# Kernel optimization log

Measured on AMD Instinct MI355X. Metric: run time of the kernel, lower is better.

Reference implementation:

```python
import jax, jax.numpy as jnp
import numpy as np

N, E, DIN, DOUT = 30000, 480000, 512, 512


def setup_inputs() -> dict:
    key = jax.random.key(0)
    ks = jax.random.split(key, 20)
    inp = {}
    inp["x"] = jax.random.normal(ks[0], (N, DIN), jnp.float32)
    inp["edge_index"] = jax.random.randint(ks[1], (2, E), 0, N, dtype=jnp.int64)
    inp["edge_weight"] = jax.random.uniform(ks[2], (E,), jnp.float32)
    sc = 1.0 / np.sqrt(DIN)
    sl = 1.0 / np.sqrt(2 * DOUT)
    for i, g in enumerate(["i", "f", "g", "o"]):
        inp[f"Wc_{g}"] = jax.random.normal(ks[3 + 4 * i], (DIN, DOUT), jnp.float32) * sc
        inp[f"bc_{g}"] = jnp.zeros((DOUT,), jnp.float32)
        inp[f"Wl_{g}"] = jax.random.normal(ks[4 + 4 * i], (2 * DOUT, DOUT), jnp.float32) * sl
        inp[f"bl_{g}"] = jnp.zeros((DOUT,), jnp.float32)
    return inp


def _gcn_norm(src, dst, w, n):
    # add self loops with weight 1.0 (improved=False), then symmetric normalization
    loops = jnp.arange(n, dtype=src.dtype)
    src = jnp.concatenate([src, loops])
    dst = jnp.concatenate([dst, loops])
    w = jnp.concatenate([w, jnp.ones((n,), w.dtype)])
    deg = jax.ops.segment_sum(w, dst, num_segments=n)
    dinv = jnp.where(deg > 0, jax.lax.rsqrt(jnp.where(deg > 0, deg, 1.0)), 0.0)
    norm = dinv[src] * w * dinv[dst]
    return src, dst, norm


def reference(x, edge_index, edge_weight,
              Wc_i, bc_i, Wl_i, bl_i,
              Wc_f, bc_f, Wl_f, bl_f,
              Wc_g, bc_g, Wl_g, bl_g,
              Wc_o, bc_o, Wl_o, bl_o):
    n = x.shape[0]
    src, dst, norm = _gcn_norm(edge_index[0], edge_index[1], edge_weight, n)
    H = jnp.zeros((n, DOUT), x.dtype)  # _set_hidden_state default
    C = jnp.zeros((n, DOUT), x.dtype)  # _set_cell_state default

    def conv(Wc, bc):
        xw = x @ Wc                                        # [N, DOUT] dense GEMM
        agg = jax.ops.segment_sum(norm[:, None] * xw[src], dst, num_segments=n)
        return agg + bc

    def gate(Wc, bc, Wl, bl, act):
        z = jnp.concatenate([conv(Wc, bc), H], axis=1)      # [N, 2*DOUT]
        return act(z @ Wl + bl)

    I = gate(Wc_i, bc_i, Wl_i, bl_i, jax.nn.sigmoid)
    F = gate(Wc_f, bc_f, Wl_f, bl_f, jax.nn.sigmoid)
    G = gate(Wc_g, bc_g, Wl_g, bl_g, jnp.tanh)
    O = gate(Wc_o, bc_o, Wl_o, bl_o, jax.nn.sigmoid)
    Cn = F * C + I * G
    Hn = O * jnp.tanh(Cn)
    return O, Hn, Cn
```

## Files before the change

kernel.cpp:

```cpp
#include <hip/hip_runtime.h>
#include <stdint.h>

typedef __bf16 bf16;
typedef __attribute__((ext_vector_type(4))) float f4;
typedef __attribute__((ext_vector_type(4))) float f32x4;
typedef __attribute__((ext_vector_type(8))) __bf16 bf8v;
typedef __attribute__((ext_vector_type(4))) __bf16 bf4v;

#define NN 30000
#define MPAD 30080
#define OUTSTRIDE 15360000

typedef __attribute__((address_space(3))) unsigned int as3_u32;
typedef __attribute__((address_space(1))) unsigned int as1_u32;

__device__ __forceinline__ void gl_lds16(const void* g, void* l) {
  __builtin_amdgcn_global_load_lds((as1_u32*)g, (as3_u32*)l, 16, 0, 0);
}

__global__ void k_init(float* deg, int* counts, int* cursor, int n) {
  int i = blockIdx.x * 256 + threadIdx.x;
  if (i < n) { deg[i] = 1.0f; counts[i] = 0; cursor[i] = 0; }
}

__global__ void k_pre(const int* __restrict__ ei, const float* __restrict__ ew,
                      float* __restrict__ deg, int* __restrict__ counts, int E) {
  int e = blockIdx.x * 256 + threadIdx.x;
  if (e < E) {
    int d = ei[E + e];
    atomicAdd(&deg[d], ew[e]);
    atomicAdd(&counts[d], 1);
  }
}

__global__ void k_dinv(float* dinv, int n) {
  int i = blockIdx.x * 256 + threadIdx.x;
  if (i < n) { float d = dinv[i]; dinv[i] = d > 0.f ? rsqrtf(d) : 0.f; }
}

__global__ void k_bsum(const int* __restrict__ counts, int* __restrict__ bsum, int n) {
  __shared__ int sm[256];
  int i = blockIdx.x * 256 + threadIdx.x;
  sm[threadIdx.x] = (i < n) ? counts[i] : 0;
  __syncthreads();
  for (int st = 128; st > 0; st >>= 1) {
    if (threadIdx.x < st) sm[threadIdx.x] += sm[threadIdx.x + st];
    __syncthreads();
  }
  if (threadIdx.x == 0) bsum[blockIdx.x] = sm[0];
}

__global__ void k_bscan(int* bsum, int nb) {
  __shared__ int buf[128];
  int t = threadIdx.x;
  int v = (t < nb) ? bsum[t] : 0;
  buf[t] = v;
  __syncthreads();
  for (int s = 1; s < 128; s <<= 1) {
    int u = (t >= s) ? buf[t - s] : 0;
    __syncthreads();
    buf[t] += u;
    __syncthreads();
  }
  if (t < nb) bsum[t] = buf[t] - v;
}

__global__ void k_offs(const int* __restrict__ counts, const int* __restrict__ bsum,
                       int* __restrict__ offs, int n, int E) {
  __shared__ int buf[256];
  int i = blockIdx.x * 256 + threadIdx.x;
  int v = (i < n) ? counts[i] : 0;
  buf[threadIdx.x] = v;
  __syncthreads();
  for (int s = 1; s < 256; s <<= 1) {
    int u = (threadIdx.x >= s) ? buf[threadIdx.x - s] : 0;
    __syncthreads();
    buf[threadIdx.x] += u;
    __syncthreads();
  }
  if (i < n) offs[i] = bsum[blockIdx.x] + buf[threadIdx.x] - v;
  if (i == 0) offs[n] = E;
}

__global__ void k_scatter(const int* __restrict__ ei, const float* __restrict__ ew,
                          const float* __restrict__ dinv, const int* __restrict__ offs,
                          int* __restrict__ cursor, int* __restrict__ srcs,
                          float* __restrict__ norms, int E) {
  int e = blockIdx.x * 256 + threadIdx.x;
  if (e >= E) return;
  int s = ei[e], d = ei[E + e];
  int pos = offs[d] + atomicAdd(&cursor[d], 1);
  srcs[pos] = s;
  norms[pos] = dinv[s] * ew[e] * dinv[d];
}

__global__ void k_xbf(const float* __restrict__ x, bf16* __restrict__ xbf, int n8) {
  int i = blockIdx.x * 256 + threadIdx.x;
  if (i >= n8) return;
  const f4* x4 = (const f4*)x;
  f4 a = x4[2 * i], b = x4[2 * i + 1];
  bf8v o;
#pragma unroll
  for (int j = 0; j < 4; ++j) { o[j] = (bf16)a[j]; o[4 + j] = (bf16)b[j]; }
  ((bf8v*)xbf)[i] = o;
}

__global__ __launch_bounds__(256) void k_agg(const int* __restrict__ offs, const int* __restrict__ srcs,
                                             const float* __restrict__ norms, const float* __restrict__ x,
                                             const float* __restrict__ dinv, const bf16* __restrict__ xbf,
                                             bf16* __restrict__ ybf) {
  int wv = (blockIdx.x * 256 + threadIdx.x) >> 6;
  int lane = threadIdx.x & 63;
  if (wv >= MPAD) return;
  bf16* yrow = ybf + ((size_t)wv << 9) + lane * 8;
  if (wv >= NN) {
    bf8v z;
#pragma unroll
    for (int j = 0; j < 8; ++j) z[j] = (bf16)0.f;
    *(bf8v*)yrow = z;
    return;
  }
  float acc[8];
  float s0 = dinv[wv]; s0 *= s0;
  const f4* xr = (const f4*)(x + ((size_t)wv << 9)) + lane * 2;
  f4 a = xr[0], b = xr[1];
#pragma unroll
  for (int j = 0; j < 4; ++j) { acc[j] = s0 * a[j]; acc[4 + j] = s0 * b[j]; }
  int e = offs[wv], end = offs[wv + 1];
  for (; e + 2 <= end; e += 2) {
    int s1 = srcs[e], s2 = srcs[e + 1];
    float n1 = norms[e], n2 = norms[e + 1];
    bf8v v1 = *(const bf8v*)(xbf + ((size_t)s1 << 9) + lane * 8);
    bf8v v2 = *(const bf8v*)(xbf + ((size_t)s2 << 9) + lane * 8);
#pragma unroll
    for (int j = 0; j < 8; ++j) acc[j] += n1 * (float)v1[j] + n2 * (float)v2[j];
  }
  if (e < end) {
    int s1 = srcs[e]; float n1 = norms[e];
    bf8v v1 = *(const bf8v*)(xbf + ((size_t)s1 << 9) + lane * 8);
#pragma unroll
    for (int j = 0; j < 8; ++j) acc[j] += n1 * (float)v1[j];
  }
  bf8v o;
#pragma unroll
  for (int j = 0; j < 8; ++j) o[j] = (bf16)acc[j];
  *(bf8v*)yrow = o;
}

__global__ void k_wcomb(const float* __restrict__ WcA, const float* __restrict__ WlA,
                        const float* __restrict__ WcB, const float* __restrict__ WlB,
                        const float* __restrict__ WcC, const float* __restrict__ WlC,
                        bf16* __restrict__ Wt) {
  const float* Wc; const float* Wl;
  int g = blockIdx.z;
  if (g == 0)      { Wc = WcA; Wl = WlA; }
  else if (g == 1) { Wc = WcB; Wl = WlB; }
  else             { Wc = WcC; Wl = WlC; }
  int k0 = blockIdx.x * 64, j0 = blockIdx.y * 64;
  int t = threadIdx.x, tx = t & 15, ty = t >> 4;
  __shared__ float sWc[64][17];
  __shared__ float sWl[16][64];
  float acc[4][4] = {};
  for (int c0 = 0; c0 < 512; c0 += 16) {
    { int kk = t >> 2, c4 = (t & 3) * 4;
      f4 v = *(const f4*)(Wc + (size_t)(k0 + kk) * 512 + c0 + c4);
#pragma unroll
      for (int j = 0; j < 4; ++j) sWc[kk][c4 + j] = v[j]; }
    { int cc = t >> 4, j4 = (t & 15) * 4;
      f4 v = *(const f4*)(Wl + (size_t)(c0 + cc) * 512 + j0 + j4);
      *(f4*)&sWl[cc][j4] = v; }
    __syncthreads();
#pragma unroll
    for (int cc = 0; cc < 16; ++cc) {
      float wcv[4], wlv[4];
#pragma unroll
      for (int b = 0; b < 4; ++b) wcv[b] = sWc[tx * 4 + b][cc];
#pragma unroll
      for (int a = 0; a < 4; ++a) wlv[a] = sWl[cc][ty * 4 + a];
#pragma unroll
      for (int a = 0; a < 4; ++a)
#pragma unroll
        for (int b = 0; b < 4; ++b) acc[a][b] += wlv[a] * wcv[b];
    }
    __syncthreads();
  }
#pragma unroll
  for (int a = 0; a < 4; ++a) {
    bf4v o;
#pragma unroll
    for (int b = 0; b < 4; ++b) o[b] = (bf16)acc[a][b];
    *(bf4v*)&Wt[((size_t)g * 512 + j0 + ty * 4 + a) * 512 + k0 + tx * 4] = o;
  }
}

__global__ void k_bcomb3(const float* __restrict__ bcA, const float* __restrict__ blA, const float* __restrict__ WlA,
                         const float* __restrict__ bcB, const float* __restrict__ blB, const float* __restrict__ WlB,
                         const float* __restrict__ bcC, const float* __restrict__ blC, const float* __restrict__ WlC,
                         float* __restrict__ bcomb) {
  int g = blockIdx.x >> 3, jc = blockIdx.x & 7;
  const float* bc; const float* bl; const float* Wl;
  if (g == 0)      { bc = bcA; bl = blA; Wl = WlA; }
  else if (g == 1) { bc = bcB; bl = blB; Wl = WlB; }
  else             { bc = bcC; bl = blC; Wl = WlC; }
  int jl = threadIdx.x & 63, part = threadIdx.x >> 6;
  int j = jc * 64 + jl;
  float s = 0.f;
  for (int c = part * 128; c < part * 128 + 128; ++c)
    s += bc[c] * Wl[(size_t)c * 512 + j];
  __shared__ float sm[4][64];
  sm[part][jl] = s;
  __syncthreads();
  if (part == 0)
    bcomb[g * 512 + j] = bl[j] + sm[0][jl] + sm[1][jl] + sm[2][jl] + sm[3][jl];
}

__global__ __launch_bounds__(256) void k_gemm(const bf16* __restrict__ A, const bf16* __restrict__ Bt,
                                              const float* __restrict__ bcomb, float* __restrict__ out) {
  __shared__ __align__(16) char lds[81920];
  const int t = threadIdx.x, lane = t & 63, w = t >> 6;
  const int wm = w >> 1, wn = w & 1;
  const int d = blockIdx.x;
  const int s = (d & 7) * 235 + (d >> 3);
  const int m0 = (s >> 3) * 128, n0 = (s & 7) * 64;
  const int l15 = lane & 15, lhi = lane >> 4;
  f32x4 acc[3][4][2] = {};

  auto stage = [&](char* base, int ks) {
    const int k0b = ks * 128;
#pragma unroll
    for (int it = 0; it < 4; ++it) {
      int P = (((it * 4 + w) << 6) | lane) << 4;
      int r = P >> 7;
      int wl = (P & 127) ^ ((r & 7) << 4);
      gl_lds16((const char*)A + (((size_t)(m0 + r)) << 10) + k0b + wl, base + P);
    }
#pragma unroll
    for (int it = 0; it < 6; ++it) {
      int flat = it * 4 + w;
      int g = flat >> 3, q = flat & 7;
      int P = ((q << 6) | lane) << 4;
      int n = P >> 7;
      int wl = (P & 127) ^ ((n & 7) << 4);
      gl_lds16((const char*)Bt + (((size_t)(g * 512 + n0 + n)) << 10) + k0b + wl,
               base + 16384 + g * 8192 + P);
    }
  };

  auto compute = [&](const char* base) {
#pragma unroll
    for (int kh = 0; kh < 2; ++kh) {
      bf8v af[4];
#pragma unroll
      for (int mi = 0; mi < 4; ++mi) {
        int r = wm * 64 + mi * 16 + l15;
        int off = (kh * 64 + lhi * 16) ^ ((r & 7) << 4);
        af[mi] = *(const bf8v*)(base + r * 128 + off);
      }
      bf8v bfr[3][2];
#pragma unroll
      for (int g = 0; g < 3; ++g)
#pragma unroll
        for (int ni = 0; ni < 2; ++ni) {
          int n = wn * 32 + ni * 16 + l15;
          int off = (kh * 64 + lhi * 16) ^ ((n & 7) << 4);
          bfr[g][ni] = *(const bf8v*)(base + 16384 + g * 8192 + n * 128 + off);
        }
#pragma unroll
      for (int g = 0; g < 3; ++g)
#pragma unroll
        for (int mi = 0; mi < 4; ++mi)
#pragma unroll
          for (int ni = 0; ni < 2; ++ni)
            acc[g][mi][ni] = __builtin_amdgcn_mfma_f32_16x16x32_bf16(bfr[g][ni], af[mi], acc[g][mi][ni], 0, 0, 0);
    }
  };

  stage(lds, 0);
  __syncthreads();
#pragma unroll
  for (int kp = 0; kp < 4; ++kp) {
    stage(lds + 40960, 2 * kp + 1);
    compute(lds);
    __syncthreads();
    if (kp < 3) stage(lds, 2 * kp + 2);
    compute(lds + 40960);
    __syncthreads();
  }

#pragma unroll
  for (int ni = 0; ni < 2; ++ni) {
    int nb = n0 + wn * 32 + ni * 16 + lhi * 4;
    f4 bI = *(const f4*)&bcomb[nb];
    f4 bG = *(const f4*)&bcomb[512 + nb];
    f4 bO = *(const f4*)&bcomb[1024 + nb];
#pragma unroll
    for (int mi = 0; mi < 4; ++mi) {
      int row = m0 + wm * 64 + mi * 16 + l15;
      if (row < NN) {
        f4 vO, vH, vC;
#pragma unroll
        for (int r = 0; r < 4; ++r) {
          float zi = acc[0][mi][ni][r] + bI[r];
          float zg = acc[1][mi][ni][r] + bG[r];
          float zo = acc[2][mi][ni][r] + bO[r];
          float I = 1.f / (1.f + __expf(-zi));
          float e2g = __expf(2.f * zg);
          float G = (e2g - 1.f) / (e2g + 1.f);
          float O = 1.f / (1.f + __expf(-zo));
          float Cn = I * G;
          float e2c = __expf(2.f * Cn);
          float tc = (e2c - 1.f) / (e2c + 1.f);
          vO[r] = O; vH[r] = O * tc; vC[r] = Cn;
        }
        size_t base = ((size_t)row << 9) + nb;
        *(f4*)&out[base] = vO;
        *(f4*)&out[OUTSTRIDE + base] = vH;
        *(f4*)&out[2 * OUTSTRIDE + base] = vC;
      }
    }
  }
}

extern "C" void kernel_launch(void* const* d_in, const int* in_sizes, int n_in,
                              void* d_out, int out_size, void* d_ws, size_t ws_size,
                              hipStream_t stream) {
  const float* x   = (const float*)d_in[0];
  const int*   ei  = (const int*)d_in[1];
  const float* ew  = (const float*)d_in[2];
  const float* Wc_i = (const float*)d_in[3];
  const float* bc_i = (const float*)d_in[4];
  const float* Wl_i = (const float*)d_in[5];
  const float* bl_i = (const float*)d_in[6];
  const float* Wc_g = (const float*)d_in[11];
  const float* bc_g = (const float*)d_in[12];
  const float* Wl_g = (const float*)d_in[13];
  const float* bl_g = (const float*)d_in[14];
  const float* Wc_o = (const float*)d_in[15];
  const float* bc_o = (const float*)d_in[16];
  const float* Wl_o = (const float*)d_in[17];
  const float* bl_o = (const float*)d_in[18];

  const int E = in_sizes[2];
  const int n = in_sizes[0] / 512;
  const int NB = (n + 255) / 256;

  char* ws = (char*)d_ws;
  bf16*  ybf   = (bf16*)ws;
  float* dinv  = (float*)(ws + 30801920);
  bf16*  Wt    = (bf16*)(ws + 30924800);
  float* bcomb = (float*)(ws + 32497664);
  int*   bsum  = (int*)(ws + 32503808);
  (void)ws_size;

  char* ob = (char*)d_out;
  float* out   = (float*)d_out;
  bf16*  xbf   = (bf16*)ob;
  int*   srcs  = (int*)(ob + 30720000);
  float* norms = (float*)(ob + 32640000);
  int*   cnts  = (int*)(ob + 34560000);
  int*   offs  = (int*)(ob + 34680000);
  int*   curs  = (int*)(ob + 34800016);
  (void)out_size; (void)n_in;

  k_init<<<NB, 256, 0, stream>>>(dinv, cnts, curs, n);
  k_pre<<<(E + 255) / 256, 256, 0, stream>>>(ei, ew, dinv, cnts, E);
  k_dinv<<<NB, 256, 0, stream>>>(dinv, n);
  k_bsum<<<NB, 256, 0, stream>>>(cnts, bsum, n);
  k_bscan<<<1, 128, 0, stream>>>(bsum, NB);
  k_offs<<<NB, 256, 0, stream>>>(cnts, bsum, offs, n, E);
  k_scatter<<<(E + 255) / 256, 256, 0, stream>>>(ei, ew, dinv, offs, curs, srcs, norms, E);
  k_xbf<<<(n * 512 / 8 + 255) / 256, 256, 0, stream>>>(x, xbf, n * 512 / 8);
  k_agg<<<(MPAD * 64 + 255) / 256, 256, 0, stream>>>(offs, srcs, norms, x, dinv, xbf, ybf);
  k_wcomb<<<dim3(8, 8, 3), 256, 0, stream>>>(Wc_i, Wl_i, Wc_g, Wl_g, Wc_o, Wl_o, Wt);
  k_bcomb3<<<24, 256, 0, stream>>>(bc_i, bl_i, Wl_i, bc_g, bl_g, Wl_g, bc_o, bl_o, Wl_o, bcomb);
  k_gemm<<<1880, 256, 0, stream>>>(ybf, Wt, bcomb, out);
}
```

Baseline: 326.8 us.

## Deepen GEMM prefetch with vmcnt waits, fuse dinv into bsum, read self term as bf16

The GEMM main loop now keeps two stages of global-to-LDS loads in flight. It uses explicit s_waitcnt vmcnt counts and raw s_barriers with sched_barriers, so the loads for tile k+2 overlap the compute on tile k. Separately, the rsqrt degree normalization is folded into the block-sum kernel to remove one launch. The aggregation self-loop term now reads the bf16 copy of x instead of fp32, which halves that read but adds rounding to the self contribution. The hand-set vmcnt value depends on how many loads each stage issues; if that count is wrong, the kernel can race.

```diff
diff --git a/kernel.cpp b/kernel.cpp
--- a/kernel.cpp
+++ b/kernel.cpp
@@ -33,15 +33,12 @@
   }
 }
 
-__global__ void k_dinv(float* dinv, int n) {
-  int i = blockIdx.x * 256 + threadIdx.x;
-  if (i < n) { float d = dinv[i]; dinv[i] = d > 0.f ? rsqrtf(d) : 0.f; }
-}
-
-__global__ void k_bsum(const int* __restrict__ counts, int* __restrict__ bsum, int n) {
+__global__ void k_bsum(const int* __restrict__ counts, int* __restrict__ bsum,
+                       float* __restrict__ dinv, int n) {
   __shared__ int sm[256];
   int i = blockIdx.x * 256 + threadIdx.x;
   sm[threadIdx.x] = (i < n) ? counts[i] : 0;
+  if (i < n) { float d = dinv[i]; dinv[i] = d > 0.f ? rsqrtf(d) : 0.f; }
   __syncthreads();
   for (int st = 128; st > 0; st >>= 1) {
     if (threadIdx.x < st) sm[threadIdx.x] += sm[threadIdx.x + st];
@@ -106,7 +103,7 @@
 }
 
 __global__ __launch_bounds__(256) void k_agg(const int* __restrict__ offs, const int* __restrict__ srcs,
-                                             const float* __restrict__ norms, const float* __restrict__ x,
+                                             const float* __restrict__ norms,
                                              const float* __restrict__ dinv, const bf16* __restrict__ xbf,
                                              bf16* __restrict__ ybf) {
   int wv = (blockIdx.x * 256 + threadIdx.x) >> 6;
@@ -122,10 +119,9 @@
   }
   float acc[8];
   float s0 = dinv[wv]; s0 *= s0;
-  const f4* xr = (const f4*)(x + ((size_t)wv << 9)) + lane * 2;
-  f4 a = xr[0], b = xr[1];
-#pragma unroll
-  for (int j = 0; j < 4; ++j) { acc[j] = s0 * a[j]; acc[4 + j] = s0 * b[j]; }
+  bf8v xv0 = *(const bf8v*)(xbf + ((size_t)wv << 9) + lane * 8);
+#pragma unroll
+  for (int j = 0; j < 8; ++j) acc[j] = s0 * (float)xv0[j];
   int e = offs[wv], end = offs[wv + 1];
   for (; e + 2 <= end; e += 2) {
     int s1 = srcs[e], s2 = srcs[e + 1];
@@ -276,15 +272,19 @@
   };
 
   stage(lds, 0);
-  __syncthreads();
-#pragma unroll
-  for (int kp = 0; kp < 4; ++kp) {
-    stage(lds + 40960, 2 * kp + 1);
-    compute(lds);
-    __syncthreads();
-    if (kp < 3) stage(lds, 2 * kp + 2);
-    compute(lds + 40960);
-    __syncthreads();
+  stage(lds + 40960, 1);
+#pragma unroll
+  for (int kp = 0; kp < 8; ++kp) {
+    if (kp < 7) asm volatile("s_waitcnt vmcnt(10)" ::: "memory");
+    else        asm volatile("s_waitcnt vmcnt(0)" ::: "memory");
+    __builtin_amdgcn_sched_barrier(0);
+    __builtin_amdgcn_s_barrier();
+    __builtin_amdgcn_sched_barrier(0);
+    compute((kp & 1) ? lds + 40960 : lds);
+    __builtin_amdgcn_sched_barrier(0);
+    __builtin_amdgcn_s_barrier();
+    __builtin_amdgcn_sched_barrier(0);
+    if (kp < 6) stage((kp & 1) ? lds + 40960 : lds, kp + 2);
   }
 
 #pragma unroll
@@ -364,13 +364,12 @@
 
   k_init<<<NB, 256, 0, stream>>>(dinv, cnts, curs, n);
   k_pre<<<(E + 255) / 256, 256, 0, stream>>>(ei, ew, dinv, cnts, E);
-  k_dinv<<<NB, 256, 0, stream>>>(dinv, n);
-  k_bsum<<<NB, 256, 0, stream>>>(cnts, bsum, n);
+  k_bsum<<<NB, 256, 0, stream>>>(cnts, bsum, dinv, n);
   k_bscan<<<1, 128, 0, stream>>>(bsum, NB);
   k_offs<<<NB, 256, 0, stream>>>(cnts, bsum, offs, n, E);
   k_scatter<<<(E + 255) / 256, 256, 0, stream>>>(ei, ew, dinv, offs, curs, srcs, norms, E);
   k_xbf<<<(n * 512 / 8 + 255) / 256, 256, 0, stream>>>(x, xbf, n * 512 / 8);
-  k_agg<<<(MPAD * 64 + 255) / 256, 256, 0, stream>>>(offs, srcs, norms, x, dinv, xbf, ybf);
+  k_agg<<<(MPAD * 64 + 255) / 256, 256, 0, stream>>>(offs, srcs, norms, dinv, xbf, ybf);
   k_wcomb<<<dim3(8, 8, 3), 256, 0, stream>>>(Wc_i, Wl_i, Wc_g, Wl_g, Wc_o, Wl_o, Wt);
   k_bcomb3<<<24, 256, 0, stream>>>(bc_i, bl_i, Wl_i, bc_g, bl_g, Wl_g, bc_o, bl_o, Wl_o, bcomb);
   k_gemm<<<1880, 256, 0, stream>>>(ybf, Wt, bcomb, out);
```

New measurement: 316.4 us. 1.03x faster.
